# Performance work log

Hardware: AMD Instinct MI355X
Metric: run time of the kernel (lower is better)

Reference implementation:

```python
import jax, jax.numpy as jnp
import numpy as np

D_MODEL = 1024
NUM_SLOTS = 64
TOP_K = 8
B, T = 4, 4096


def setup_inputs() -> dict:
    key = jax.random.key(0)
    ks = jax.random.split(key, 16)
    D, S = D_MODEL, NUM_SLOTS
    H = D // 2  # route MLP hidden (hardcoded d_model//2 in source)
    sc = lambda fan_in: 1.0 / np.sqrt(fan_in)
    inp = {
        "x": jax.random.normal(ks[0], (B, T, D), dtype=jnp.float32),
        # learned params
        "slot_init": jax.random.normal(ks[1], (S, D), dtype=jnp.float32) * 0.1,
        "slot_scale": jnp.ones((S, 1), dtype=jnp.float32),
        "w1": jax.random.normal(ks[2], (H, 2 * D), dtype=jnp.float32) * sc(2 * D),
        "b1": jnp.zeros((H,), dtype=jnp.float32),
        "w2": jax.random.normal(ks[3], (S, H), dtype=jnp.float32) * sc(H),
        "b2": jnp.zeros((S,), dtype=jnp.float32),
        "gru_wih": jax.random.normal(ks[4], (3 * D, D), dtype=jnp.float32) * sc(D),
        "gru_whh": jax.random.normal(ks[5], (3 * D, D), dtype=jnp.float32) * sc(D),
        "gru_bih": jnp.zeros((3 * D,), dtype=jnp.float32),
        "gru_bhh": jnp.zeros((3 * D,), dtype=jnp.float32),
        "wv": jax.random.normal(ks[6], (D, D), dtype=jnp.float32) * sc(D),
        "bv": jnp.zeros((D,), dtype=jnp.float32),
        "wo": jax.random.normal(ks[7], (D, D), dtype=jnp.float32) * sc(D),
        "bo": jnp.zeros((D,), dtype=jnp.float32),
        "tau": jnp.ones((1,), dtype=jnp.float32),
    }
    return inp


def _forward(x, slot_init, slot_scale, w1, b1, w2, b2,
             gru_wih, gru_whh, gru_bih, gru_bhh, wv, bv, wo, bo, tau):
    Bn, Tn, D = x.shape
    Sn = slot_init.shape[0]
    # initial slot states, expanded over batch: (B, S, D)
    S = jnp.broadcast_to((slot_init * slot_scale)[None], (Bn, Sn, D)).astype(x.dtype)
    slot_mean = S.mean(axis=1, keepdims=True)                      # (B,1,D)
    ctx = jnp.concatenate([x, jnp.broadcast_to(slot_mean, x.shape)], axis=-1)  # (B,T,2D)
    h = jax.nn.gelu(ctx @ w1.T + b1, approximate=False)
    route_logits = (h @ w2.T + b2) / (jnp.abs(tau) + 0.1)          # (B,T,S)
    topk_vals, topk_idx = jax.lax.top_k(route_logits, TOP_K)
    topk_w = jax.nn.softmax(topk_vals, axis=-1)                    # (B,T,K)
    # scatter top-k weights into dense alpha (B,T,S)
    alpha = jnp.sum(topk_w[..., None] * jax.nn.one_hot(topk_idx, Sn, dtype=x.dtype), axis=-2)
    slot_input = jnp.einsum('bts,btd->bsd', alpha, x)              # dispatch
    slot_wsum = alpha.sum(axis=1) + 1e-8                           # (B,S)
    gi = (slot_input / slot_wsum[..., None]).reshape(Bn * Sn, D)
    hs = S.reshape(Bn * Sn, D)
    # GRUCell (torch semantics)
    gx = gi @ gru_wih.T + gru_bih                                  # (BS, 3D)
    gh = hs @ gru_whh.T + gru_bhh
    xr, xz, xn = jnp.split(gx, 3, axis=-1)
    hr, hz, hn = jnp.split(gh, 3, axis=-1)
    r = jax.nn.sigmoid(xr + hr)
    z = jax.nn.sigmoid(xz + hz)
    n = jnp.tanh(xn + r * hn)
    h_new = (1.0 - z) * n + z * hs
    S_new = h_new.reshape(Bn, Sn, D)
    slot_values = S_new @ wv.T + bv                                # (B,S,D)
    out = jnp.einsum('bts,bsd->btd', alpha, slot_values)           # combine
    return out @ wo.T + bo


def reference(x, slot_init, slot_scale, w1, b1, w2, b2,
              gru_wih, gru_whh, gru_bih, gru_bhh, wv, bv, wo, bo, tau):
    return _forward(x, slot_init, slot_scale, w1, b1, w2, b2,
                    gru_wih, gru_whh, gru_bih, gru_bhh, wv, bv, wo, bo, tau)
```

## Files before the change

kernel.cpp:

```cpp
#include <hip/hip_runtime.h>

using u16 = unsigned short;
using u32 = unsigned int;

typedef __attribute__((ext_vector_type(8))) short bf16x8;
typedef __attribute__((ext_vector_type(4))) float f32x4;

#define NTOK 16384

constexpr size_t OFF_FLAG   = 0;
constexpr size_t OFF_FCNT   = 256;
constexpr size_t OFF_M      = 512;
constexpr size_t OFF_B1P64  = 8704;
constexpr size_t OFF_B1P32  = 12800;
constexpr size_t OFF_B2F    = 14848;
constexpr size_t OFF_BIHF   = 15104;
constexpr size_t OFF_BHHF   = 27392;
constexpr size_t OFF_BVF    = 39680;
constexpr size_t OFF_BOF    = 43776;
constexpr size_t OFF_FLAGS  = 47872;
constexpr size_t OFF_HSHI   = 113408;
constexpr size_t OFF_HSLO   = 244480;
constexpr size_t OFF_HSF    = 375552;
constexpr size_t OFF_GH     = 637696;
constexpr size_t OFF_GIHI   = 1424128;
constexpr size_t OFF_GILO   = 1948416;
constexpr size_t OFF_GX     = 2472704;
constexpr size_t OFF_SNHI   = 5618432;
constexpr size_t OFF_SNLO   = 6142720;
constexpr size_t OFF_SVHI   = 6667008;
constexpr size_t OFF_SVLO   = 7191296;
constexpr size_t OFF_SVO    = 7715584;
constexpr size_t OFF_IDX    = 8764160;
constexpr size_t OFF_WGT    = 9288448;
constexpr size_t OFF_LOGITS = 9812736;
constexpr size_t OFF_W1HI   = 14007040;
constexpr size_t OFF_W1LO   = 16104192;
constexpr size_t OFF_W2HI   = 18201344;
constexpr size_t OFF_W2LO   = 18266880;
constexpr size_t OFF_WIHHI  = 18332416;
constexpr size_t OFF_WIHLO  = 24623872;
constexpr size_t OFF_WHHHI  = 30915328;
constexpr size_t OFF_WHHLO  = 37206784;
constexpr size_t OFF_WVHI   = 43498240;
constexpr size_t OFF_WVLO   = 45595392;
constexpr size_t OFF_WOHI   = 47692544;
constexpr size_t OFF_WOLO   = 49789696;
constexpr size_t OFF_HHI    = 51886848;
constexpr size_t OFF_HLO    = 68664064;
constexpr size_t OFF_DPART  = 85441280;
constexpr size_t OFF_DWSUM  = 93829888;
constexpr size_t WS_NEED    = 93838080;

__device__ __forceinline__ float bf2f(u16 u) {
  union { u32 i; float f; } c; c.i = ((u32)u) << 16; return c.f;
}
__device__ __forceinline__ u16 f2bf(float f) {
  u32 x = __float_as_uint(f);
  x += 0x7fffu + ((x >> 16) & 1u);
  return (u16)(x >> 16);
}
__device__ __forceinline__ void splitf(float v, u16& hi, u16& lo) {
  hi = f2bf(v);
  lo = f2bf(v - bf2f(hi));
}
__device__ __forceinline__ float rdval(const void* p, int i, int f32m) {
  return f32m ? ((const float*)p)[i] : bf2f(((const u16*)p)[i]);
}
__device__ __forceinline__ void async16(const u16* g, u16* l) {
  __builtin_amdgcn_global_load_lds((const __attribute__((address_space(1))) void*)g,
                                   (__attribute__((address_space(3))) void*)l, 16, 0, 0);
}

__global__ void k_sniff(const u32* __restrict__ w1w, int* __restrict__ flag) {
  int t = threadIdx.x;
  u32 word = w1w[t * 97];
  int ef = (word >> 7) & 0xFF;
  unsigned long long m = __ballot(ef >= 128);
  if (t == 0) flag[0] = (__popcll(m) >= 8) ? 1 : 0;
}

__global__ __launch_bounds__(256) void k_cvt_all(
    const void* __restrict__ w1, const void* __restrict__ w2,
    const void* __restrict__ wih, const void* __restrict__ whh,
    const void* __restrict__ wv, const void* __restrict__ wo,
    const void* __restrict__ b2, const void* __restrict__ bih,
    const void* __restrict__ bhh, const void* __restrict__ bv,
    const void* __restrict__ bo, char* __restrict__ ws,
    const int* __restrict__ flagp)
{
  const int f = *flagp;
  const long long gid = (long long)blockIdx.x * 256 + threadIdx.x;
  const long long C0 = 1048576, C1 = C0 + 32768, C2 = C1 + 3145728,
                  C3 = C2 + 3145728, C4 = C3 + 1048576, C5 = C4 + 1048576;
  if (gid < C5) {
    const void* src; size_t oh, ol; int i;
    if (gid < C0)      { src = w1;  oh = OFF_W1HI;  ol = OFF_W1LO;  i = (int)gid; }
    else if (gid < C1) { src = w2;  oh = OFF_W2HI;  ol = OFF_W2LO;  i = (int)(gid - C0); }
    else if (gid < C2) { src = wih; oh = OFF_WIHHI; ol = OFF_WIHLO; i = (int)(gid - C1); }
    else if (gid < C3) { src = whh; oh = OFF_WHHHI; ol = OFF_WHHLO; i = (int)(gid - C2); }
    else if (gid < C4) { src = wv;  oh = OFF_WVHI;  ol = OFF_WVLO;  i = (int)(gid - C3); }
    else               { src = wo;  oh = OFF_WOHI;  ol = OFF_WOLO;  i = (int)(gid - C4); }
    float v = rdval(src, i, f);
    u16 hi, lo; splitf(v, hi, lo);
    ((u16*)(ws + oh))[i] = hi;
    ((u16*)(ws + ol))[i] = lo;
    return;
  }
  int r = (int)(gid - C5);
  if (r >= 8256) return;
  const void* src; size_t od; int i;
  if (r < 64)        { src = b2;  od = OFF_B2F;  i = r; }
  else if (r < 3136) { src = bih; od = OFF_BIHF; i = r - 64; }
  else if (r < 6208) { src = bhh; od = OFF_BHHF; i = r - 3136; }
  else if (r < 7232) { src = bv;  od = OFF_BVF;  i = r - 6208; }
  else               { src = bo;  od = OFF_BOF;  i = r - 7232; }
  ((float*)(ws + od))[i] = rdval(src, i, f);
}

template<int MODE>
__global__ __launch_bounds__(512, 2) void gemm_bt(
    const u16* __restrict__ Ahi, const u16* __restrict__ Alo,
    const u16* __restrict__ Bhi, const u16* __restrict__ Blo,
    int M, int N, int K, int ldb,
    const float* __restrict__ biasF, float* __restrict__ outF,
    u16* __restrict__ outHi, u16* __restrict__ outLo)
{
  __shared__ alignas(16) u16 smem[2 * 2 * 8192];
  const int t    = threadIdx.x;
  const int grp  = t >> 8;
  const int tl   = t & 255;
  const int wvid = tl >> 6;
  const int lane = t & 63;
  const int quad = lane >> 4;
  const int l16  = lane & 15;
  const int row0 = blockIdx.x * 128;
  const int col0 = blockIdx.y * 128;
  const int wr   = (wvid >> 1) * 64;
  const int wc   = (wvid & 1) * 64;

  const int ra  = tl >> 2;
  const int kqe = (tl & 3) * 8;
  int r_a0 = row0 + ra;      if (r_a0 > M - 1) r_a0 = M - 1;
  int r_a1 = row0 + ra + 64; if (r_a1 > M - 1) r_a1 = M - 1;
  int r_b0 = col0 + ra;      if (r_b0 > N - 1) r_b0 = N - 1;
  int r_b1 = col0 + ra + 64; if (r_b1 > N - 1) r_b1 = N - 1;
  const size_t aoff0 = (size_t)r_a0 * K + kqe;
  const size_t aoff1 = (size_t)r_a1 * K + kqe;
  const size_t boff0 = (size_t)r_b0 * ldb + kqe;
  const size_t boff1 = (size_t)r_b1 * ldb + kqe;

  const int KH  = K >> 1;
  const int NIT = 3 * (KH >> 5);
  int sp = 0, sk = grp * KH;
  const int skend = grp * KH + KH;

  u16* const base = smem + grp * 16384;
  auto stage = [&](int buf) {
    const u16* Ap = (sp == 1) ? Alo : Ahi;
    const u16* Bp = (sp == 2) ? Blo : Bhi;
    u16* At = base + buf * 8192;
    u16* Bt = At + 4096;
    async16(Ap + aoff0 + sk, &At[(wvid * 64) * 8]);
    async16(Ap + aoff1 + sk, &At[(wvid * 64 + 256) * 8]);
    async16(Bp + boff0 + sk, &Bt[(wvid * 64) * 8]);
    async16(Bp + boff1 + sk, &Bt[(wvid * 64 + 256) * 8]);
    sk += 32;
    if (sk == skend) { sk = grp * KH; ++sp; }
  };

  f32x4 acc[4][4] = {};
  stage(0);
  asm volatile("s_waitcnt vmcnt(0)" ::: "memory");
  __syncthreads();
  int cur = 0;
  for (int it = 0; it < NIT; ++it) {
    if (it + 1 < NIT) stage(cur ^ 1);
    const u16* At = base + cur * 8192;
    const u16* Bt = At + 4096;
    bf16x8 af[4], bfr[4];
    #pragma unroll
    for (int mt = 0; mt < 4; ++mt)
      af[mt] = *(const bf16x8*)&At[(wr + mt * 16 + l16) * 32 + quad * 8];
    #pragma unroll
    for (int nt = 0; nt < 4; ++nt)
      bfr[nt] = *(const bf16x8*)&Bt[(wc + nt * 16 + l16) * 32 + quad * 8];
    #pragma unroll
    for (int mt = 0; mt < 4; ++mt)
      #pragma unroll
      for (int nt = 0; nt < 4; ++nt)
        acc[mt][nt] = __builtin_amdgcn_mfma_f32_16x16x32_bf16(
            af[mt], bfr[nt], acc[mt][nt], 0, 0, 0);
    asm volatile("s_waitcnt vmcnt(0)" ::: "memory");
    __syncthreads();
    cur ^= 1;
  }

  float* red = (float*)smem;
  #pragma unroll 1
  for (int half = 0; half < 2; ++half) {
    if (grp == 1 && (wvid & 1) == half) {
      #pragma unroll
      for (int mt = 0; mt < 4; ++mt)
        #pragma unroll
        for (int nt = 0; nt < 4; ++nt)
          #pragma unroll
          for (int r2 = 0; r2 < 4; ++r2)
            red[(wr + mt * 16 + quad * 4 + r2) * 64 + nt * 16 + l16] =
                acc[mt][nt][r2];
    }
    __syncthreads();
    if (grp == 0 && (wvid & 1) == half) {
      #pragma unroll
      for (int mt = 0; mt < 4; ++mt)
        #pragma unroll
        for (int nt = 0; nt < 4; ++nt)
          #pragma unroll
          for (int r2 = 0; r2 < 4; ++r2)
            acc[mt][nt][r2] +=
                red[(wr + mt * 16 + quad * 4 + r2) * 64 + nt * 16 + l16];
    }
    __syncthreads();
  }
  if (grp != 0) return;

  #pragma unroll
  for (int mt = 0; mt < 4; ++mt) {
    #pragma unroll
    for (int nt = 0; nt < 4; ++nt) {
      const int col = col0 + wc + nt * 16 + l16;
      if (col >= N) continue;
      #pragma unroll
      for (int r2 = 0; r2 < 4; ++r2) {
        const int row = row0 + wr + mt * 16 + quad * 4 + r2;
        if (row >= M) continue;
        float v = acc[mt][nt][r2] + biasF[col];
        size_t idx = (size_t)row * N + col;
        if constexpr (MODE == 0) {
          outF[idx] = v;
        } else {
          u16 hi, lo; splitf(v, hi, lo);
          outHi[idx] = hi; outLo[idx] = lo;
        }
      }
    }
  }
}

__global__ __launch_bounds__(256, 4) void gemm_router(
    const void* __restrict__ X,
    const u16* __restrict__ Bhi, const u16* __restrict__ Blo,
    int M, int N, int K, int ldb, const float* __restrict__ biasF,
    u16* __restrict__ outHi, u16* __restrict__ outLo,
    const int* __restrict__ flagp)
{
  __shared__ alignas(16) u16 Athi[64 * 32];
  __shared__ alignas(16) u16 Atlo[64 * 32];
  __shared__ alignas(16) u16 Bthi[128 * 32];
  __shared__ alignas(16) u16 Btlo[128 * 32];
  const int f32m = *flagp;
  const int t    = threadIdx.x;
  const int wvid = t >> 6;
  const int lane = t & 63;
  const int quad = lane >> 4;
  const int l16  = lane & 15;
  const int row0 = blockIdx.x * 64;
  const int col0 = blockIdx.y * 128;
  const int wr   = (wvid >> 1) * 32;
  const int wc   = (wvid & 1) * 64;

  const int ra  = t >> 2;
  const int kqe = (t & 3) * 8;
  int r_b0 = col0 + ra;      if (r_b0 > N - 1) r_b0 = N - 1;
  int r_b1 = col0 + ra + 64; if (r_b1 > N - 1) r_b1 = N - 1;
  const u16* gBhi0 = Bhi + (size_t)r_b0 * ldb + kqe;
  const u16* gBhi1 = Bhi + (size_t)r_b1 * ldb + kqe;
  const u16* gBlo0 = Blo + (size_t)r_b0 * ldb + kqe;
  const u16* gBlo1 = Blo + (size_t)r_b1 * ldb + kqe;
  const float* Xf = (const float*)X;
  const u16*   Xb = (const u16*)X;

  f32x4 acc[2][4] = {};

  for (int k0 = 0; k0 < K; k0 += 32) {
    async16(gBhi0 + k0, &Bthi[(wvid * 64) * 8]);
    async16(gBhi1 + k0, &Bthi[(wvid * 64 + 256) * 8]);
    async16(gBlo0 + k0, &Btlo[(wvid * 64) * 8]);
    async16(gBlo1 + k0, &Btlo[(wvid * 64 + 256) * 8]);
    #pragma unroll
    for (int i = 0; i < 2; ++i) {
      int j = t + 256 * i;
      int row = j >> 3, kq = (j & 7) * 4;
      int grow = row0 + row; if (grow > M - 1) grow = M - 1;
      ushort4 hi4, lo4;
      if (f32m) {
        const float4 v = *(const float4*)(Xf + (size_t)grow * K + k0 + kq);
        splitf(v.x, hi4.x, lo4.x);
        splitf(v.y, hi4.y, lo4.y);
        splitf(v.z, hi4.z, lo4.z);
        splitf(v.w, hi4.w, lo4.w);
      } else {
        hi4 = *(const ushort4*)(Xb + (size_t)grow * K + k0 + kq);
        lo4.x = lo4.y = lo4.z = lo4.w = 0;
      }
      *(ushort4*)&Athi[row * 32 + kq] = hi4;
      *(ushort4*)&Atlo[row * 32 + kq] = lo4;
    }
    asm volatile("s_waitcnt vmcnt(0)" ::: "memory");
    __syncthreads();
    bf16x8 ah[2], al[2], bh[4], bl[4];
    #pragma unroll
    for (int mt = 0; mt < 2; ++mt) {
      ah[mt] = *(const bf16x8*)&Athi[(wr + mt * 16 + l16) * 32 + quad * 8];
      al[mt] = *(const bf16x8*)&Atlo[(wr + mt * 16 + l16) * 32 + quad * 8];
    }
    #pragma unroll
    for (int nt = 0; nt < 4; ++nt) {
      bh[nt] = *(const bf16x8*)&Bthi[(wc + nt * 16 + l16) * 32 + quad * 8];
      bl[nt] = *(const bf16x8*)&Btlo[(wc + nt * 16 + l16) * 32 + quad * 8];
    }
    #pragma unroll
    for (int mt = 0; mt < 2; ++mt)
      #pragma unroll
      for (int nt = 0; nt < 4; ++nt) {
        acc[mt][nt] = __builtin_amdgcn_mfma_f32_16x16x32_bf16(
            ah[mt], bh[nt], acc[mt][nt], 0, 0, 0);
        acc[mt][nt] = __builtin_amdgcn_mfma_f32_16x16x32_bf16(
            al[mt], bh[nt], acc[mt][nt], 0, 0, 0);
        acc[mt][nt] = __builtin_amdgcn_mfma_f32_16x16x32_bf16(
            ah[mt], bl[nt], acc[mt][nt], 0, 0, 0);
      }
    __syncthreads();
  }

  #pragma unroll
  for (int mt = 0; mt < 2; ++mt) {
    #pragma unroll
    for (int nt = 0; nt < 4; ++nt) {
      const int col = col0 + wc + nt * 16 + l16;
      if (col >= N) continue;
      #pragma unroll
      for (int r2 = 0; r2 < 4; ++r2) {
        const int row = row0 + wr + mt * 16 + quad * 4 + r2;
        if (row >= M) continue;
        float v = acc[mt][nt][r2] + biasF[col];
        v = 0.5f * v * (1.0f + erff(v * 0.70710678118654752f));
        u16 hi, lo; splitf(v, hi, lo);
        size_t idx = (size_t)row * N + col;
        outHi[idx] = hi; outLo[idx] = lo;
      }
    }
  }
}

__global__ __launch_bounds__(256) void k_init(const void* __restrict__ sli,
    const void* __restrict__ slsc, const int* __restrict__ flagp,
    double* __restrict__ m64, int* __restrict__ fcnt,
    u16* __restrict__ hshi, u16* __restrict__ hslo, float* __restrict__ hsf)
{
  int f = *flagp;
  int gid = blockIdx.x * 256 + threadIdx.x;
  if (gid == 0) fcnt[0] = 0;
  if (gid < 1024) {
    double s = 0.0;
    for (int j = 0; j < 64; ++j)
      s += (double)rdval(sli, j * 1024 + gid, f) * (double)rdval(slsc, j, f);
    m64[gid] = s * (1.0 / 64.0);
  }
  for (int i = gid; i < 64 * 1024; i += 16384) {
    int s = i >> 10;
    float v = rdval(sli, i, f) * rdval(slsc, s, f);
    splitf(v, hshi[i], hslo[i]);
    hsf[i] = v;
  }
}

__global__ __launch_bounds__(256) void k_b1p(const void* __restrict__ w1,
    const void* __restrict__ b1, const int* __restrict__ flagp,
    const double* __restrict__ m64, double* __restrict__ b1p64,
    float* __restrict__ b1p32)
{
  int f = *flagp;
  int h = blockIdx.x * 256 + threadIdx.x;
  if (h >= 512) return;
  double a = (double)rdval(b1, h, f);
  if (f) {
    const float* wr = (const float*)w1 + (size_t)h * 2048 + 1024;
    for (int d = 0; d < 1024; ++d) a += (double)wr[d] * m64[d];
  } else {
    const u16* wr = (const u16*)w1 + (size_t)h * 2048 + 1024;
    for (int d = 0; d < 1024; ++d) a += (double)bf2f(wr[d]) * m64[d];
  }
  b1p64[h] = a;
  b1p32[h] = (float)a;
}

__global__ __launch_bounds__(256) void k_topk(const float* __restrict__ logits,
    const void* __restrict__ tau, const int* __restrict__ flagp,
    int* __restrict__ idxb, float* __restrict__ wgtb,
    int* __restrict__ fcnt, int* __restrict__ flags)
{
  const int f32m = *flagp;
  const int n    = blockIdx.x * 4 + (threadIdx.x >> 6);
  const int lane = threadIdx.x & 63;
  float cur = logits[(size_t)n * 64 + lane];
  float tv[8]; int ti[8]; float v9 = 0.f;
  #pragma unroll
  for (int it = 0; it < 9; ++it) {
    float v = cur; int i = lane;
    #pragma unroll
    for (int off = 32; off; off >>= 1) {
      float ov = __shfl_xor(v, off);
      int   oi = __shfl_xor(i, off);
      if (ov > v || (ov == v && oi < i)) { v = ov; i = oi; }
    }
    if (it < 8) { tv[it] = v; ti[it] = i; if (lane == i) cur = -__builtin_inff(); }
    else v9 = v;
  }
  float itau = 1.0f / (fabsf(rdval(tau, 0, f32m)) + 0.1f);
  float e[8], z = 0.f;
  #pragma unroll
  for (int k = 0; k < 8; ++k) { e[k] = expf((tv[k] - tv[0]) * itau); z += e[k]; }
  if (lane == 0) {
    float theta = f32m ? 2e-4f : 1e-4f;
    if (tv[7] - v9 < theta) { int p = atomicAdd(fcnt, 1); flags[p] = n; }
    float rz = 1.0f / z;
    #pragma unroll
    for (int k = 0; k < 8; ++k) {
      idxb[n * 8 + k] = ti[k];
      wgtb[n * 8 + k] = e[k] * rz;
    }
  }
}

__global__ __launch_bounds__(256) void k_repair(const void* __restrict__ x,
    const void* __restrict__ w1, const void* __restrict__ w2,
    const void* __restrict__ b2, const void* __restrict__ tau,
    const int* __restrict__ flagp, const double* __restrict__ b1p64,
    const int* __restrict__ fcnt, const int* __restrict__ flags,
    int* __restrict__ idxb, float* __restrict__ wgtb)
{
  __shared__ double hsm[512];
  __shared__ double lg[64];
  const int f = *flagp;
  const int cnt = *fcnt;
  const int t = threadIdx.x;
  for (int q = blockIdx.x; q < cnt; q += gridDim.x) {
    const int n = flags[q];
    for (int h = t; h < 512; h += 256) {
      double a = b1p64[h];
      if (f) {
        const float* xr = (const float*)x + (size_t)n * 1024;
        const float* wr = (const float*)w1 + (size_t)h * 2048;
        for (int d = 0; d < 1024; ++d) a += (double)xr[d] * (double)wr[d];
      } else {
        const u16* xr = (const u16*)x + (size_t)n * 1024;
        const u16* wr = (const u16*)w1 + (size_t)h * 2048;
        for (int d = 0; d < 1024; ++d) a += (double)bf2f(xr[d]) * (double)bf2f(wr[d]);
      }
      hsm[h] = 0.5 * a * (1.0 + erf(a * 0.70710678118654752440));
    }
    __syncthreads();
    if (t < 64) {
      double a = (double)rdval(b2, t, f);
      if (f) {
        const float* wr = (const float*)w2 + (size_t)t * 512;
        for (int k = 0; k < 512; ++k) a += hsm[k] * (double)wr[k];
      } else {
        const u16* wr = (const u16*)w2 + (size_t)t * 512;
        for (int k = 0; k < 512; ++k) a += hsm[k] * (double)bf2f(wr[k]);
      }
      lg[t] = a;
    }
    __syncthreads();
    if (t == 0) {
      double tv = fabs((double)rdval(tau, 0, f)) + 0.1;
      double vals[8]; int ids[8];
      for (int it = 0; it < 8; ++it) {
        double best = -1e300; int bi = 0;
        for (int i = 0; i < 64; ++i)
          if (lg[i] > best) { best = lg[i]; bi = i; }
        vals[it] = best; ids[it] = bi; lg[bi] = -1e300;
      }
      double e[8], z = 0.0;
      for (int k = 0; k < 8; ++k) { e[k] = exp((vals[k] - vals[0]) / tv); z += e[k]; }
      for (int k = 0; k < 8; ++k) {
        idxb[n * 8 + k] = ids[k];
        wgtb[n * 8 + k] = (float)(e[k] / z);
      }
    }
    __syncthreads();
  }
}

__global__ __launch_bounds__(256) void k_dispatch(const void* __restrict__ X,
    const int* __restrict__ flagp, const int* __restrict__ idxb,
    const float* __restrict__ wgtb,
    float* __restrict__ dpart, float* __restrict__ dwsum)
{
  __shared__ int   ltok[512];
  __shared__ float lw[512];
  __shared__ int   lcnt;
  __shared__ float lws;
  const int f32m = *flagp;
  const int g    = blockIdx.x;
  const int xcd  = g & 7;
  const int ord  = g >> 3;
  const int win  = xcd * 4 + (ord >> 6);
  const int s    = ord & 63;
  const int b     = win >> 3;
  const int chunk = win & 7;
  const int t     = threadIdx.x;
  if (t == 0) { lcnt = 0; lws = 0.f; }
  __syncthreads();
  const int tok0 = b * 4096 + chunk * 512;
  float mysum = 0.f;
  for (int tok = tok0 + t; tok < tok0 + 512; tok += 256) {
    int hit = -1;
    #pragma unroll
    for (int k = 0; k < 8; ++k)
      if (idxb[(size_t)tok * 8 + k] == s) hit = k;
    if (hit >= 0) {
      float w = wgtb[(size_t)tok * 8 + hit];
      int p = atomicAdd(&lcnt, 1);
      ltok[p] = tok; lw[p] = w;
      mysum += w;
    }
  }
  atomicAdd(&lws, mysum);
  __syncthreads();
  const int cnt = lcnt;
  float a0 = 0.f, a1 = 0.f, a2 = 0.f, a3 = 0.f;
  if (f32m) {
    const float* Xf = (const float*)X;
    for (int e = 0; e < cnt; ++e) {
      int tok = ltok[e]; float w = lw[e];
      const float4 v = *(const float4*)(Xf + (size_t)tok * 1024 + 4 * t);
      a0 += w * v.x; a1 += w * v.y; a2 += w * v.z; a3 += w * v.w;
    }
  } else {
    const u16* Xb = (const u16*)X;
    for (int e = 0; e < cnt; ++e) {
      int tok = ltok[e]; float w = lw[e];
      const ushort4 v = *(const ushort4*)(Xb + (size_t)tok * 1024 + 4 * t);
      a0 += w * bf2f(v.x); a1 += w * bf2f(v.y);
      a2 += w * bf2f(v.z); a3 += w * bf2f(v.w);
    }
  }
  const int bs = b * 64 + s;
  float* pp = dpart + ((size_t)bs * 8 + chunk) * 1024 + 4 * t;
  float4 outv = { a0, a1, a2, a3 };
  *(float4*)pp = outv;
  if (t == 0) dwsum[bs * 8 + chunk] = lws;
}

__global__ __launch_bounds__(256) void k_dreduce(const float* __restrict__ dpart,
    const float* __restrict__ dwsum, u16* __restrict__ gihi, u16* __restrict__ gilo)
{
  const int bs = blockIdx.x;
  const int t  = threadIdx.x;
  float ws = 0.f;
  #pragma unroll
  for (int c = 0; c < 8; ++c) ws += dwsum[bs * 8 + c];
  const float inv = 1.0f / (ws + 1e-8f);
  float a0 = 0.f, a1 = 0.f, a2 = 0.f, a3 = 0.f;
  const float* pb = dpart + (size_t)bs * 8 * 1024 + 4 * t;
  #pragma unroll
  for (int c = 0; c < 8; ++c) {
    const float4 v = *(const float4*)(pb + c * 1024);
    a0 += v.x; a1 += v.y; a2 += v.z; a3 += v.w;
  }
  const size_t base = (size_t)bs * 1024 + 4 * t;
  splitf(a0 * inv, gihi[base + 0], gilo[base + 0]);
  splitf(a1 * inv, gihi[base + 1], gilo[base + 1]);
  splitf(a2 * inv, gihi[base + 2], gilo[base + 2]);
  splitf(a3 * inv, gihi[base + 3], gilo[base + 3]);
}

__global__ __launch_bounds__(256) void k_gru(const float* __restrict__ gx,
    const float* __restrict__ gh, const float* __restrict__ hsf,
    u16* __restrict__ snhi, u16* __restrict__ snlo)
{
  int gid = blockIdx.x * 256 + threadIdx.x;
  int r = gid >> 10, d = gid & 1023, s = r & 63;
  const float* gxr = gx + (size_t)r * 3072;
  const float* ghr = gh + (size_t)s * 3072;
  float rr = 1.0f / (1.0f + expf(-(gxr[d] + ghr[d])));
  float zz = 1.0f / (1.0f + expf(-(gxr[1024 + d] + ghr[1024 + d])));
  float nn = tanhf(gxr[2048 + d] + rr * ghr[2048 + d]);
  float hs = hsf[s * 1024 + d];
  float hv = (1.0f - zz) * nn + zz * hs;
  splitf(hv, snhi[gid], snlo[gid]);
}

__global__ __launch_bounds__(256) void k_out(const int* __restrict__ idxb,
    const float* __restrict__ wgtb, const float* __restrict__ svo,
    const int* __restrict__ flagp, void* __restrict__ out)
{
  const int f32m = *flagp;
  int n = blockIdx.x * 4 + (threadIdx.x >> 6);
  int lane = threadIdx.x & 63;
  int b = n >> 12;
  const float* svb = svo + (size_t)b * 64 * 1024;
  int id[8]; float w[8];
  #pragma unroll
  for (int k = 0; k < 8; ++k) { id[k] = idxb[n * 8 + k]; w[k] = wgtb[n * 8 + k]; }
  #pragma unroll
  for (int i = 0; i < 16; ++i) {
    int d = i * 64 + lane;
    float a = 0.f;
    #pragma unroll
    for (int k = 0; k < 8; ++k) a += w[k] * svb[(size_t)id[k] * 1024 + d];
    size_t idx = (size_t)n * 1024 + d;
    if (f32m) ((float*)out)[idx] = a;
    else      ((u16*)out)[idx] = f2bf(a);
  }
}

extern "C" void kernel_launch(void* const* d_in, const int* in_sizes, int n_in,
                              void* d_out, int out_size, void* d_ws, size_t ws_size,
                              hipStream_t stream) {
  if (ws_size < WS_NEED) {
    hipMemsetAsync(d_out, 0, (size_t)out_size * 2, stream);
    return;
  }
  const void* x    = d_in[0];
  const void* sli  = d_in[1];
  const void* slsc = d_in[2];
  const void* w1   = d_in[3];
  const void* b1   = d_in[4];
  const void* w2   = d_in[5];
  const void* b2   = d_in[6];
  const void* wih  = d_in[7];
  const void* whh  = d_in[8];
  const void* bih  = d_in[9];
  const void* bhh  = d_in[10];
  const void* wv   = d_in[11];
  const void* bv   = d_in[12];
  const void* wo   = d_in[13];
  const void* bo   = d_in[14];
  const void* tau  = d_in[15];
  char* ws = (char*)d_ws;

  int*    flag   = (int*)(ws + OFF_FLAG);
  int*    fcnt   = (int*)(ws + OFF_FCNT);
  double* m64    = (double*)(ws + OFF_M);
  double* b1p64  = (double*)(ws + OFF_B1P64);
  float*  b1p32  = (float*)(ws + OFF_B1P32);
  float*  b2f    = (float*)(ws + OFF_B2F);
  float*  bihf   = (float*)(ws + OFF_BIHF);
  float*  bhhf   = (float*)(ws + OFF_BHHF);
  float*  bvf    = (float*)(ws + OFF_BVF);
  float*  bof    = (float*)(ws + OFF_BOF);
  int*    flags  = (int*)(ws + OFF_FLAGS);
  u16*    hshi   = (u16*)(ws + OFF_HSHI);
  u16*    hslo   = (u16*)(ws + OFF_HSLO);
  float*  hsf    = (float*)(ws + OFF_HSF);
  float*  gh     = (float*)(ws + OFF_GH);
  u16*    gihi   = (u16*)(ws + OFF_GIHI);
  u16*    gilo   = (u16*)(ws + OFF_GILO);
  float*  gx     = (float*)(ws + OFF_GX);
  u16*    snhi   = (u16*)(ws + OFF_SNHI);
  u16*    snlo   = (u16*)(ws + OFF_SNLO);
  u16*    svhi   = (u16*)(ws + OFF_SVHI);
  u16*    svlo   = (u16*)(ws + OFF_SVLO);
  float*  svo    = (float*)(ws + OFF_SVO);
  int*    idxb   = (int*)(ws + OFF_IDX);
  float*  wgtb   = (float*)(ws + OFF_WGT);
  float*  logits = (float*)(ws + OFF_LOGITS);
  u16*    w1hi   = (u16*)(ws + OFF_W1HI);
  u16*    w1lo   = (u16*)(ws + OFF_W1LO);
  u16*    w2hi   = (u16*)(ws + OFF_W2HI);
  u16*    w2lo   = (u16*)(ws + OFF_W2LO);
  u16*    wihhi  = (u16*)(ws + OFF_WIHHI);
  u16*    wihlo  = (u16*)(ws + OFF_WIHLO);
  u16*    whhhi  = (u16*)(ws + OFF_WHHHI);
  u16*    whhlo  = (u16*)(ws + OFF_WHHLO);
  u16*    wvhi   = (u16*)(ws + OFF_WVHI);
  u16*    wvlo   = (u16*)(ws + OFF_WVLO);
  u16*    wohi   = (u16*)(ws + OFF_WOHI);
  u16*    wolo   = (u16*)(ws + OFF_WOLO);
  u16*    hhi    = (u16*)(ws + OFF_HHI);
  u16*    hlo    = (u16*)(ws + OFF_HLO);
  float*  dpart  = (float*)(ws + OFF_DPART);
  float*  dwsum  = (float*)(ws + OFF_DWSUM);

  k_sniff<<<1, 64, 0, stream>>>((const u32*)w1, flag);

  k_init<<<64, 256, 0, stream>>>(sli, slsc, flag, m64, fcnt, hshi, hslo, hsf);
  k_b1p<<<2, 256, 0, stream>>>(w1, b1, flag, m64, b1p64, b1p32);

  k_cvt_all<<<37025, 256, 0, stream>>>(w1, w2, wih, whh, wv, wo,
                                       b2, bih, bhh, bv, bo, ws, flag);

  gemm_bt<0><<<dim3(1, 24), 512, 0, stream>>>(
      hshi, hslo, whhhi, whhlo, 64, 3072, 1024, 1024, bhhf, gh, nullptr, nullptr);

  gemm_router<<<dim3(256, 4), 256, 0, stream>>>(
      x, w1hi, w1lo, NTOK, 512, 1024, 2048, b1p32, hhi, hlo, flag);

  gemm_bt<0><<<dim3(128, 1), 512, 0, stream>>>(
      hhi, hlo, w2hi, w2lo, NTOK, 64, 512, 512, b2f, logits, nullptr, nullptr);

  k_topk<<<4096, 256, 0, stream>>>(logits, tau, flag, idxb, wgtb, fcnt, flags);
  k_repair<<<1024, 256, 0, stream>>>(x, w1, w2, b2, tau, flag, b1p64, fcnt, flags,
                                     idxb, wgtb);
  k_dispatch<<<2048, 256, 0, stream>>>(x, flag, idxb, wgtb, dpart, dwsum);
  k_dreduce<<<256, 256, 0, stream>>>(dpart, dwsum, gihi, gilo);

  gemm_bt<0><<<dim3(2, 24), 512, 0, stream>>>(
      gihi, gilo, wihhi, wihlo, 256, 3072, 1024, 1024, bihf, gx, nullptr, nullptr);

  k_gru<<<1024, 256, 0, stream>>>(gx, gh, hsf, snhi, snlo);

  gemm_bt<3><<<dim3(2, 8), 512, 0, stream>>>(
      snhi, snlo, wvhi, wvlo, 256, 1024, 1024, 1024, bvf, nullptr, svhi, svlo);

  gemm_bt<0><<<dim3(2, 8), 512, 0, stream>>>(
      svhi, svlo, wohi, wolo, 256, 1024, 1024, 1024, bof, svo, nullptr, nullptr);

  k_out<<<4096, 256, 0, stream>>>(idxb, wgtb, svo, flag, d_out);

  (void)in_sizes; (void)n_in; (void)out_size; (void)ws_size;
}
```

Baseline: 757.4 us.

## Split router repair into parallel hidden-layer and top-k kernels with wave reductions

The fp64 repair of near-tie tokens is split in two. A new kernel computes the hidden GELU layer for up to 256 flagged tokens, spreading each token over 8 blocks with coalesced per-lane loads and wave shuffle reductions, and stores the results in a workspace buffer. A second kernel reads those hidden values back, computes the 64 logits with wave-parallel dot products instead of one thread per slot, and then does the exact top-k. This targets the serial per-thread 1024-long dot products of the old repair kernel, at the cost of an extra launch, extra workspace and a fallback path for tokens past the cap.

```diff
diff --git a/kernel.cpp b/kernel.cpp
--- a/kernel.cpp
+++ b/kernel.cpp
@@ -50,7 +50,10 @@
 constexpr size_t OFF_HLO    = 68664064;
 constexpr size_t OFF_DPART  = 85441280;
 constexpr size_t OFF_DWSUM  = 93829888;
-constexpr size_t WS_NEED    = 93838080;
+constexpr size_t OFF_HSMG   = 93838080;
+constexpr size_t WS_NEED    = 94886656;
+
+constexpr int QCAP = 256;
 
 __device__ __forceinline__ float bf2f(u16 u) {
   union { u32 i; float f; } c; c.i = ((u32)u) << 16; return c.f;
@@ -433,44 +436,130 @@
   }
 }
 
-__global__ __launch_bounds__(256) void k_repair(const void* __restrict__ x,
+__global__ __launch_bounds__(256) void k_repair_h(const void* __restrict__ x,
+    const void* __restrict__ w1, const int* __restrict__ flagp,
+    const double* __restrict__ b1p64, const int* __restrict__ fcnt,
+    const int* __restrict__ flags, double* __restrict__ hsmg)
+{
+  const int f = *flagp;
+  int cnt = *fcnt; if (cnt > QCAP) cnt = QCAP;
+  const int q = blockIdx.x >> 3;
+  if (q >= cnt) return;
+  const int chunk = blockIdx.x & 7;
+  const int n  = flags[q];
+  const int wv = threadIdx.x >> 6;
+  const int lane = threadIdx.x & 63;
+
+  float xr[16];
+  if (f) {
+    const float* xp = (const float*)x + (size_t)n * 1024;
+    #pragma unroll
+    for (int j = 0; j < 16; ++j) xr[j] = xp[lane + 64 * j];
+  } else {
+    const u16* xp = (const u16*)x + (size_t)n * 1024;
+    #pragma unroll
+    for (int j = 0; j < 16; ++j) xr[j] = bf2f(xp[lane + 64 * j]);
+  }
+
+  const int h0 = chunk * 64 + wv * 16;
+  for (int r = 0; r < 16; ++r) {
+    const int h = h0 + r;
+    double a0 = 0.0, a1 = 0.0;
+    if (f) {
+      const float* wr = (const float*)w1 + (size_t)h * 2048;
+      #pragma unroll
+      for (int j = 0; j < 16; j += 2) {
+        a0 += (double)xr[j]     * (double)wr[lane + 64 * j];
+        a1 += (double)xr[j + 1] * (double)wr[lane + 64 * (j + 1)];
+      }
+    } else {
+      const u16* wr = (const u16*)w1 + (size_t)h * 2048;
+      #pragma unroll
+      for (int j = 0; j < 16; j += 2) {
+        a0 += (double)xr[j]     * (double)bf2f(wr[lane + 64 * j]);
+        a1 += (double)xr[j + 1] * (double)bf2f(wr[lane + 64 * (j + 1)]);
+      }
+    }
+    double a = a0 + a1;
+    #pragma unroll
+    for (int off = 32; off; off >>= 1) a += __shfl_xor(a, off);
+    if (lane == 0) {
+      a += b1p64[h];
+      hsmg[(size_t)q * 512 + h] =
+          0.5 * a * (1.0 + erf(a * 0.70710678118654752440));
+    }
+  }
+}
+
+__global__ __launch_bounds__(256) void k_repair_t(const void* __restrict__ x,
     const void* __restrict__ w1, const void* __restrict__ w2,
     const void* __restrict__ b2, const void* __restrict__ tau,
     const int* __restrict__ flagp, const double* __restrict__ b1p64,
     const int* __restrict__ fcnt, const int* __restrict__ flags,
-    int* __restrict__ idxb, float* __restrict__ wgtb)
+    const double* __restrict__ hsmg, int* __restrict__ idxb,
+    float* __restrict__ wgtb)
 {
   __shared__ double hsm[512];
   __shared__ double lg[64];
   const int f = *flagp;
   const int cnt = *fcnt;
   const int t = threadIdx.x;
+  const int wv = t >> 6;
+  const int lane = t & 63;
   for (int q = blockIdx.x; q < cnt; q += gridDim.x) {
     const int n = flags[q];
-    for (int h = t; h < 512; h += 256) {
-      double a = b1p64[h];
+    if (q < QCAP) {
+      for (int h = t; h < 512; h += 256) hsm[h] = hsmg[(size_t)q * 512 + h];
+    } else {
+      for (int h = wv; h < 512; h += 4) {
+        double a0 = 0.0, a1 = 0.0;
+        if (f) {
+          const float* xp = (const float*)x + (size_t)n * 1024;
+          const float* wr = (const float*)w1 + (size_t)h * 2048;
+          for (int j = 0; j < 16; j += 2) {
+            a0 += (double)xp[lane + 64 * j]       * (double)wr[lane + 64 * j];
+            a1 += (double)xp[lane + 64 * (j + 1)] * (double)wr[lane + 64 * (j + 1)];
+          }
+        } else {
+          const u16* xp = (const u16*)x + (size_t)n * 1024;
+          const u16* wr = (const u16*)w1 + (size_t)h * 2048;
+          for (int j = 0; j < 16; j += 2) {
+            a0 += (double)bf2f(xp[lane + 64 * j]) * (double)bf2f(wr[lane + 64 * j]);
+            a1 += (double)bf2f(xp[lane + 64 * (j + 1)]) *
+                  (double)bf2f(wr[lane + 64 * (j + 1)]);
+          }
+        }
+        double a = a0 + a1;
+        #pragma unroll
+        for (int off = 32; off; off >>= 1) a += __shfl_xor(a, off);
+        if (lane == 0) {
+          a += b1p64[h];
+          hsm[h] = 0.5 * a * (1.0 + erf(a * 0.70710678118654752440));
+        }
+      }
+    }
+    __syncthreads();
+    for (int s = wv; s < 64; s += 4) {
+      double a0 = 0.0, a1 = 0.0;
       if (f) {
-        const float* xr = (const float*)x + (size_t)n * 1024;
-        const float* wr = (const float*)w1 + (size_t)h * 2048;
-        for (int d = 0; d < 1024; ++d) a += (double)xr[d] * (double)wr[d];
+        const float* wr = (const float*)w2 + (size_t)s * 512;
+        #pragma unroll
+        for (int j = 0; j < 8; j += 2) {
+          a0 += hsm[lane + 64 * j]       * (double)wr[lane + 64 * j];
+          a1 += hsm[lane + 64 * (j + 1)] * (double)wr[lane + 64 * (j + 1)];
+        }
       } else {
-        const u16* xr = (const u16*)x + (size_t)n * 1024;
-        const u16* wr = (const u16*)w1 + (size_t)h * 2048;
-        for (int d = 0; d < 1024; ++d) a += (double)bf2f(xr[d]) * (double)bf2f(wr[d]);
-      }
-      hsm[h] = 0.5 * a * (1.0 + erf(a * 0.70710678118654752440));
-    }
-    __syncthreads();
-    if (t < 64) {
-      double a = (double)rdval(b2, t, f);
-      if (f) {
-        const float* wr = (const float*)w2 + (size_t)t * 512;
-        for (int k = 0; k < 512; ++k) a += hsm[k] * (double)wr[k];
-      } else {
-        const u16* wr = (const u16*)w2 + (size_t)t * 512;
-        for (int k = 0; k < 512; ++k) a += hsm[k] * (double)bf2f(wr[k]);
-      }
-      lg[t] = a;
+        const u16* wr = (const u16*)w2 + (size_t)s * 512;
+        #pragma unroll
+        for (int j = 0; j < 8; j += 2) {
+          a0 += hsm[lane + 64 * j]       * (double)bf2f(wr[lane + 64 * j]);
+          a1 += hsm[lane + 64 * (j + 1)] * (double)bf2f(wr[lane + 64 * (j + 1)]);
+        }
+      }
+      double a = a0 + a1;
+      #pragma unroll
+      for (int off = 32; off; off >>= 1) a += __shfl_xor(a, off);
+      if (lane == 0) lg[s] = a + (double)rdval(b2, s, f);
     }
     __syncthreads();
     if (t == 0) {
@@ -684,6 +773,7 @@
   u16*    hlo    = (u16*)(ws + OFF_HLO);
   float*  dpart  = (float*)(ws + OFF_DPART);
   float*  dwsum  = (float*)(ws + OFF_DWSUM);
+  double* hsmg   = (double*)(ws + OFF_HSMG);
 
   k_sniff<<<1, 64, 0, stream>>>((const u32*)w1, flag);
 
@@ -703,8 +793,9 @@
       hhi, hlo, w2hi, w2lo, NTOK, 64, 512, 512, b2f, logits, nullptr, nullptr);
 
   k_topk<<<4096, 256, 0, stream>>>(logits, tau, flag, idxb, wgtb, fcnt, flags);
-  k_repair<<<1024, 256, 0, stream>>>(x, w1, w2, b2, tau, flag, b1p64, fcnt, flags,
-                                     idxb, wgtb);
+  k_repair_h<<<2048, 256, 0, stream>>>(x, w1, flag, b1p64, fcnt, flags, hsmg);
+  k_repair_t<<<256, 256, 0, stream>>>(x, w1, w2, b2, tau, flag, b1p64, fcnt,
+                                      flags, hsmg, idxb, wgtb);
   k_dispatch<<<2048, 256, 0, stream>>>(x, flag, idxb, wgtb, dpart, dwsum);
   k_dreduce<<<256, 256, 0, stream>>>(dpart, dwsum, gihi, gilo);
 
```

New measurement: 664.0 us. -12.3%, faster.
